# Performance work log

Measured on AMD Instinct MI355X. Metric: run time of the kernel, lower is better.

## Reference

```python
import jax, jax.numpy as jnp
import numpy as np


def setup_inputs() -> dict:
    key = jax.random.key(0)
    k1, k2, k3, k4 = jax.random.split(key, 4)
    B, T, S, D = 256, 16, 32, 768
    return {
        "video_global": jax.random.normal(k1, (B, D), dtype=jnp.float32),
        "text_global": jax.random.normal(k2, (B, D), dtype=jnp.float32),
        "video_local": jax.random.normal(k3, (B, T, D), dtype=jnp.float32),
        "text_local": jax.random.normal(k4, (B, S, D), dtype=jnp.float32),
        "temp": jnp.zeros((1,), dtype=jnp.float32),  # log(1.0)
    }


def reference(video_global, text_global, video_local, text_local, temp):
    B = video_global.shape[0]
    logit_scale = jnp.exp(temp)[0]

    # ---- global contrastive loss ----
    global_sim = logit_scale * (video_global @ text_global.T)  # [B, B]
    diag = jnp.arange(B)
    loss_v2t = -jax.nn.log_softmax(global_sim, axis=1)[diag, diag].mean()
    loss_t2v = -jax.nn.log_softmax(global_sim, axis=0)[diag, diag].mean()
    loss_global = 0.5 * (loss_v2t + loss_t2v)

    # ---- local positive scores ----
    # paired (diagonal) local similarity: [B, T, S]
    sim_pos = logit_scale * jnp.einsum("btd,bsd->bts", video_local, text_local)
    time_weights = jax.nn.softmax(sim_pos.max(axis=-1), axis=-1)  # [B, T]
    pos_scores = (sim_pos.mean(axis=-1) * time_weights).sum(axis=1)  # [B]

    # ---- local negative scores (batched pairwise contraction) ----
    # [B, B, T, S]: video i vs text j, replacing the B*(B-1) tiny einsum loop
    sim_all = logit_scale * jnp.einsum("btd,csd->bcts", video_local, text_local)
    neg_full = (time_weights[:, None, :] * sim_all.mean(axis=-1)).sum(axis=-1)  # [B, B]

    # drop diagonal (i == j), preserving row-major loop order
    rows, cols = np.nonzero(~np.eye(B, dtype=bool))
    neg_scores = neg_full[rows, cols].reshape(B, B - 1)

    logits = jnp.concatenate([pos_scores[:, None], neg_scores], axis=-1)  # [B, B]
    loss_local = -jax.nn.log_softmax(logits, axis=-1)[:, 0].mean()

    return 0.6 * loss_global + 0.4 * loss_local
```

## Files before the change

### kernel.cpp

```cpp
#include <hip/hip_runtime.h>
#include <cmath>

#define BB 256
#define TT 16
#define SS 32
#define DD 768
#define LROW 260

__global__ __launch_bounds__(256) void hl_stage1(
    const float* __restrict__ vl, const float* __restrict__ tl,
    const float* __restrict__ temp,
    float* __restrict__ vw_ws, float* __restrict__ tb_ws)
{
    __shared__ float smem[12480];
    const int i   = blockIdx.x;
    const int tid = threadIdx.x;
    const float lsc = expf(temp[0]);

    const int slice = tid >> 4;
    const int tpos  = (tid >> 2) & 3;
    const int spos  = tid & 3;

    const float* vli = vl + (size_t)i * TT * DD;
    const float* tli = tl + (size_t)i * SS * DD;

    float acc[4][8];
#pragma unroll
    for (int a0 = 0; a0 < 4; ++a0)
#pragma unroll
        for (int b0 = 0; b0 < 8; ++b0) acc[a0][b0] = 0.f;

    for (int c = 0; c < 3; ++c) {
        const int d0 = c << 8;
#pragma unroll
        for (int k = 0; k < 4; ++k) {
            int f4 = tid + (k << 8);
            int r  = f4 >> 6;
            int dc = (f4 << 2) & 255;
            *(float4*)&smem[r * LROW + dc] =
                *(const float4*)&vli[r * DD + d0 + dc];
        }
#pragma unroll
        for (int k = 0; k < 8; ++k) {
            int f4 = tid + (k << 8);
            int r  = f4 >> 6;
            int dc = (f4 << 2) & 255;
            *(float4*)&smem[(16 + r) * LROW + dc] =
                *(const float4*)&tli[r * DD + d0 + dc];
        }
        __syncthreads();
#pragma unroll
        for (int step = 0; step < 4; ++step) {
            const int db = (slice << 4) + (step << 2);
            float4 av[4];
            float4 bv[8];
#pragma unroll
            for (int ti = 0; ti < 4; ++ti)
                av[ti] = *(const float4*)&smem[(tpos * 4 + ti) * LROW + db];
#pragma unroll
            for (int sj = 0; sj < 8; ++sj)
                bv[sj] = *(const float4*)&smem[(16 + spos * 8 + sj) * LROW + db];
#pragma unroll
            for (int ti = 0; ti < 4; ++ti)
#pragma unroll
                for (int sj = 0; sj < 8; ++sj)
                    acc[ti][sj] += av[ti].x * bv[sj].x + av[ti].y * bv[sj].y
                                 + av[ti].z * bv[sj].z + av[ti].w * bv[sj].w;
        }
        __syncthreads();
    }

#pragma unroll
    for (int ti = 0; ti < 4; ++ti)
#pragma unroll
        for (int sj = 0; sj < 8; ++sj) {
            int t = tpos * 4 + ti, s = spos * 8 + sj;
            smem[(t * 32 + s) * 16 + slice] = acc[ti][sj];
        }
    __syncthreads();
    for (int rep = 0; rep < 2; ++rep) {
        int o = tid + (rep << 8);
        float ssum = 0.f;
#pragma unroll
        for (int k = 0; k < 16; ++k) ssum += smem[o * 16 + k];
        smem[8192 + o] = lsc * ssum;
    }
    __syncthreads();
    if (tid < 16) {
        float m = -3.0e38f;
        for (int s = 0; s < 32; ++s) m = fmaxf(m, smem[8192 + tid * 32 + s]);
        smem[8704 + tid] = m;
    }
    __syncthreads();
    if (tid == 0) {
        float M = -3.0e38f;
        for (int t = 0; t < 16; ++t) M = fmaxf(M, smem[8704 + t]);
        float ssum = 0.f;
        for (int t = 0; t < 16; ++t) {
            float e = expf(smem[8704 + t] - M);
            smem[8720 + t] = e;
            ssum += e;
        }
        float inv = 1.0f / ssum;
        for (int t = 0; t < 16; ++t) smem[8720 + t] *= inv;
    }
    __syncthreads();

#pragma unroll
    for (int k = 0; k < 3; ++k) {
        int d = tid + (k << 8);
        float vwv = 0.f;
#pragma unroll
        for (int t = 0; t < 16; ++t) vwv += smem[8720 + t] * vli[t * DD + d];
        vw_ws[(size_t)i * DD + d] = vwv;
        float tbv = 0.f;
#pragma unroll
        for (int s = 0; s < 32; ++s) tbv += tli[s * DD + d];
        tb_ws[(size_t)i * DD + d] = tbv * (1.0f / 32.0f);
    }
}

__global__ __launch_bounds__(256) void hl_stage2(
    const float* __restrict__ vg, const float* __restrict__ tg,
    const float* __restrict__ vw, const float* __restrict__ tb,
    const float* __restrict__ temp, float* __restrict__ out)
{
    __shared__ float a_s[4 * DD];
    __shared__ float xs[4 * 256];
    __shared__ float wred[4];
    __shared__ float bcast;

    const int tid  = threadIdx.x;
    const int mode = blockIdx.x >> 6;
    const int ib   = (blockIdx.x & 63) << 2;
    const float lsc = expf(temp[0]);

    const float* Arows;
    const float* Mat;
    float w;
    if (mode == 0)      { Arows = vw + (size_t)ib * DD; Mat = tb; w = 0.4f / 256.0f; }
    else if (mode == 1) { Arows = vg + (size_t)ib * DD; Mat = tg; w = 0.3f / 256.0f; }
    else                { Arows = tg + (size_t)ib * DD; Mat = vg; w = 0.3f / 256.0f; }

#pragma unroll
    for (int k = 0; k < 3; ++k) {
        int f4 = tid + (k << 8);
        *(float4*)&a_s[f4 << 2] = *(const float4*)&Arows[f4 << 2];
    }
    __syncthreads();

    const float4* mrow = (const float4*)(Mat + (size_t)tid * DD);
    float4 acc[4];
#pragma unroll
    for (int r = 0; r < 4; ++r) { acc[r].x = acc[r].y = acc[r].z = acc[r].w = 0.f; }

#pragma unroll 4
    for (int k = 0; k < DD / 4; ++k) {
        float4 m4 = mrow[k];
#pragma unroll
        for (int r = 0; r < 4; ++r) {
            float4 a4 = *(const float4*)&a_s[r * DD + (k << 2)];
            acc[r].x += m4.x * a4.x;
            acc[r].y += m4.y * a4.y;
            acc[r].z += m4.z * a4.z;
            acc[r].w += m4.w * a4.w;
        }
    }
#pragma unroll
    for (int r = 0; r < 4; ++r)
        xs[r * 256 + tid] = (acc[r].x + acc[r].y + acc[r].z + acc[r].w) * lsc;
    __syncthreads();

    float local = 0.f;
    for (int r = 0; r < 4; ++r) {
        float v = xs[r * 256 + tid];
        float m = v;
#pragma unroll
        for (int off = 32; off > 0; off >>= 1)
            m = fmaxf(m, __shfl_down(m, off, 64));
        if ((tid & 63) == 0) wred[tid >> 6] = m;
        __syncthreads();
        if (tid == 0)
            bcast = fmaxf(fmaxf(wred[0], wred[1]), fmaxf(wred[2], wred[3]));
        __syncthreads();
        float M = bcast;
        float e = expf(v - M);
        float ssum = e;
#pragma unroll
        for (int off = 32; off > 0; off >>= 1)
            ssum += __shfl_down(ssum, off, 64);
        if ((tid & 63) == 0) wred[tid >> 6] = ssum;
        __syncthreads();
        if (tid == 0) {
            float Stot = wred[0] + wred[1] + wred[2] + wred[3];
            float lse  = M + logf(Stot);
            local += w * (lse - xs[r * 256 + ib + r]);
        }
        __syncthreads();
    }
    if (tid == 0) atomicAdd(out, local);
}

extern "C" void kernel_launch(void* const* d_in, const int* in_sizes, int n_in,
                              void* d_out, int out_size, void* d_ws, size_t ws_size,
                              hipStream_t stream)
{
    const float* vg   = (const float*)d_in[0];
    const float* tg   = (const float*)d_in[1];
    const float* vl   = (const float*)d_in[2];
    const float* tl   = (const float*)d_in[3];
    const float* temp = (const float*)d_in[4];
    float* out = (float*)d_out;

    float* vw = (float*)d_ws;
    float* tb = vw + (size_t)BB * DD;

    hipMemsetAsync(out, 0, sizeof(float) * out_size, stream);
    hl_stage1<<<dim3(BB), dim3(256), 0, stream>>>(vl, tl, temp, vw, tb);
    hl_stage2<<<dim3(192), dim3(256), 0, stream>>>(vg, tg, vw, tb, temp, out);
}
```

Measured before the change: 125.1 us.

## Split-K tiled GEMM for global/local sims with separate LSE kernel, widen stage1

```diff
diff --git a/kernel.cpp b/kernel.cpp
--- a/kernel.cpp
+++ b/kernel.cpp
@@ -7,63 +7,65 @@
 #define DD 768
 #define LROW 260
 
-__global__ __launch_bounds__(256) void hl_stage1(
+__global__ __launch_bounds__(512) void hl_stage1(
     const float* __restrict__ vl, const float* __restrict__ tl,
     const float* __restrict__ temp,
     float* __restrict__ vw_ws, float* __restrict__ tb_ws)
 {
     __shared__ float smem[12480];
+    __shared__ float simb[512];
+    __shared__ float rmax[16];
+    __shared__ float twb[16];
+
     const int i   = blockIdx.x;
     const int tid = threadIdx.x;
     const float lsc = expf(temp[0]);
 
-    const int slice = tid >> 4;
-    const int tpos  = (tid >> 2) & 3;
-    const int spos  = tid & 3;
+    const int slice = tid & 15;
+    const int g     = tid >> 4;
+    const int tg    = g >> 3;
+    const int sg    = g & 7;
 
     const float* vli = vl + (size_t)i * TT * DD;
     const float* tli = tl + (size_t)i * SS * DD;
 
-    float acc[4][8];
-#pragma unroll
-    for (int a0 = 0; a0 < 4; ++a0)
-#pragma unroll
-        for (int b0 = 0; b0 < 8; ++b0) acc[a0][b0] = 0.f;
+    float acc[4][4];
+#pragma unroll
+    for (int a = 0; a < 4; ++a)
+#pragma unroll
+        for (int b = 0; b < 4; ++b) acc[a][b] = 0.f;
 
     for (int c = 0; c < 3; ++c) {
         const int d0 = c << 8;
 #pragma unroll
+        for (int k = 0; k < 2; ++k) {
+            int f4 = tid + (k << 9);
+            int r  = f4 >> 6;
+            int dc = (f4 & 63) << 2;
+            *(float4*)&smem[r * LROW + dc] = *(const float4*)&vli[r * DD + d0 + dc];
+        }
+#pragma unroll
         for (int k = 0; k < 4; ++k) {
-            int f4 = tid + (k << 8);
+            int f4 = tid + (k << 9);
             int r  = f4 >> 6;
-            int dc = (f4 << 2) & 255;
-            *(float4*)&smem[r * LROW + dc] =
-                *(const float4*)&vli[r * DD + d0 + dc];
-        }
-#pragma unroll
-        for (int k = 0; k < 8; ++k) {
-            int f4 = tid + (k << 8);
-            int r  = f4 >> 6;
-            int dc = (f4 << 2) & 255;
-            *(float4*)&smem[(16 + r) * LROW + dc] =
-                *(const float4*)&tli[r * DD + d0 + dc];
+            int dc = (f4 & 63) << 2;
+            *(float4*)&smem[(16 + r) * LROW + dc] = *(const float4*)&tli[r * DD + d0 + dc];
         }
         __syncthreads();
 #pragma unroll
         for (int step = 0; step < 4; ++step) {
             const int db = (slice << 4) + (step << 2);
-            float4 av[4];
-            float4 bv[8];
+            float4 av[4], bv[4];
 #pragma unroll
             for (int ti = 0; ti < 4; ++ti)
-                av[ti] = *(const float4*)&smem[(tpos * 4 + ti) * LROW + db];
-#pragma unroll
-            for (int sj = 0; sj < 8; ++sj)
-                bv[sj] = *(const float4*)&smem[(16 + spos * 8 + sj) * LROW + db];
+                av[ti] = *(const float4*)&smem[(tg * 4 + ti) * LROW + db];
+#pragma unroll
+            for (int sj = 0; sj < 4; ++sj)
+                bv[sj] = *(const float4*)&smem[(16 + sg * 4 + sj) * LROW + db];
 #pragma unroll
             for (int ti = 0; ti < 4; ++ti)
 #pragma unroll
-                for (int sj = 0; sj < 8; ++sj)
+                for (int sj = 0; sj < 4; ++sj)
                     acc[ti][sj] += av[ti].x * bv[sj].x + av[ti].y * bv[sj].y
                                  + av[ti].z * bv[sj].z + av[ti].w * bv[sj].w;
         }
@@ -73,45 +75,43 @@
 #pragma unroll
     for (int ti = 0; ti < 4; ++ti)
 #pragma unroll
-        for (int sj = 0; sj < 8; ++sj) {
-            int t = tpos * 4 + ti, s = spos * 8 + sj;
-            smem[(t * 32 + s) * 16 + slice] = acc[ti][sj];
-        }
-    __syncthreads();
-    for (int rep = 0; rep < 2; ++rep) {
-        int o = tid + (rep << 8);
+        for (int sj = 0; sj < 4; ++sj) {
+            int t = tg * 4 + ti, s = sg * 4 + sj;
+            smem[(t * 32 + s) * 17 + slice] = acc[ti][sj];
+        }
+    __syncthreads();
+    {
         float ssum = 0.f;
 #pragma unroll
-        for (int k = 0; k < 16; ++k) ssum += smem[o * 16 + k];
-        smem[8192 + o] = lsc * ssum;
+        for (int k = 0; k < 16; ++k) ssum += smem[tid * 17 + k];
+        simb[tid] = lsc * ssum;
     }
     __syncthreads();
     if (tid < 16) {
         float m = -3.0e38f;
-        for (int s = 0; s < 32; ++s) m = fmaxf(m, smem[8192 + tid * 32 + s]);
-        smem[8704 + tid] = m;
+        for (int s = 0; s < 32; ++s)
+            m = fmaxf(m, simb[tid * 32 + ((s + tid) & 31)]);
+        rmax[tid] = m;
     }
     __syncthreads();
     if (tid == 0) {
         float M = -3.0e38f;
-        for (int t = 0; t < 16; ++t) M = fmaxf(M, smem[8704 + t]);
+        for (int t = 0; t < 16; ++t) M = fmaxf(M, rmax[t]);
         float ssum = 0.f;
         for (int t = 0; t < 16; ++t) {
-            float e = expf(smem[8704 + t] - M);
-            smem[8720 + t] = e;
+            float e = expf(rmax[t] - M);
+            twb[t] = e;
             ssum += e;
         }
         float inv = 1.0f / ssum;
-        for (int t = 0; t < 16; ++t) smem[8720 + t] *= inv;
-    }
-    __syncthreads();
-
-#pragma unroll
-    for (int k = 0; k < 3; ++k) {
-        int d = tid + (k << 8);
+        for (int t = 0; t < 16; ++t) twb[t] *= inv;
+    }
+    __syncthreads();
+
+    for (int d = tid; d < DD; d += 512) {
         float vwv = 0.f;
 #pragma unroll
-        for (int t = 0; t < 16; ++t) vwv += smem[8720 + t] * vli[t * DD + d];
+        for (int t = 0; t < 16; ++t) vwv += twb[t] * vli[t * DD + d];
         vw_ws[(size_t)i * DD + d] = vwv;
         float tbv = 0.f;
 #pragma unroll
@@ -120,85 +120,124 @@
     }
 }
 
-__global__ __launch_bounds__(256) void hl_stage2(
+__global__ __launch_bounds__(256) void hl_gemm(
     const float* __restrict__ vg, const float* __restrict__ tg,
     const float* __restrict__ vw, const float* __restrict__ tb,
-    const float* __restrict__ temp, float* __restrict__ out)
-{
-    __shared__ float a_s[4 * DD];
-    __shared__ float xs[4 * 256];
+    const float* __restrict__ temp, float* __restrict__ cparts)
+{
+    __shared__ float As[16][68];
+    __shared__ float Bs[16][68];
+    __shared__ float Tb[64][68];
+
+    const int b   = blockIdx.x;
+    const int p   = b & 7;
+    const int tj  = (b >> 3) & 3;
+    const int ti  = (b >> 5) & 3;
+    const int mat = b >> 7;
+    const int tid = threadIdx.x;
+    const float lsc = expf(temp[0]);
+
+    const float* A  = mat ? vw : vg;
+    const float* Bm = mat ? tb : tg;
+    const int i0 = ti * 64, j0 = tj * 64, kb0 = p * 96;
+
+    const int srow = tid >> 2, skq = tid & 3;
+    const int tr = tid >> 4, tc = tid & 15;
+
+    float acc[4][4];
+#pragma unroll
+    for (int r = 0; r < 4; ++r)
+#pragma unroll
+        for (int cc = 0; cc < 4; ++cc) acc[r][cc] = 0.f;
+
+    for (int ch = 0; ch < 6; ++ch) {
+        const int kb = kb0 + ch * 16;
+        float4 a4 = *(const float4*)&A [(size_t)(i0 + srow) * DD + kb + skq * 4];
+        float4 b4 = *(const float4*)&Bm[(size_t)(j0 + srow) * DD + kb + skq * 4];
+        __syncthreads();
+        As[skq * 4 + 0][srow] = a4.x; As[skq * 4 + 1][srow] = a4.y;
+        As[skq * 4 + 2][srow] = a4.z; As[skq * 4 + 3][srow] = a4.w;
+        Bs[skq * 4 + 0][srow] = b4.x; Bs[skq * 4 + 1][srow] = b4.y;
+        Bs[skq * 4 + 2][srow] = b4.z; Bs[skq * 4 + 3][srow] = b4.w;
+        __syncthreads();
+#pragma unroll
+        for (int k = 0; k < 16; ++k) {
+            float4 av = *(const float4*)&As[k][tr * 4];
+            float4 bv = *(const float4*)&Bs[k][tc * 4];
+            float ar[4] = {av.x, av.y, av.z, av.w};
+            float br[4] = {bv.x, bv.y, bv.z, bv.w};
+#pragma unroll
+            for (int r = 0; r < 4; ++r)
+#pragma unroll
+                for (int cc = 0; cc < 4; ++cc)
+                    acc[r][cc] += ar[r] * br[cc];
+        }
+    }
+
+    const int cm = mat ? 0 : 1;
+    float* Cp = cparts + ((size_t)p * 3 + cm) * 65536;
+#pragma unroll
+    for (int r = 0; r < 4; ++r) {
+        float4 v = {acc[r][0] * lsc, acc[r][1] * lsc, acc[r][2] * lsc, acc[r][3] * lsc};
+        *(float4*)&Cp[(size_t)(i0 + tr * 4 + r) * 256 + j0 + tc * 4] = v;
+    }
+    if (mat == 0) {
+        __syncthreads();
+#pragma unroll
+        for (int r = 0; r < 4; ++r)
+#pragma unroll
+            for (int cc = 0; cc < 4; ++cc)
+                Tb[tc * 4 + cc][tr * 4 + r] = acc[r][cc] * lsc;
+        __syncthreads();
+        float* Ct = cparts + ((size_t)p * 3 + 2) * 65536;
+#pragma unroll
+        for (int r = 0; r < 4; ++r) {
+            float4 v = *(const float4*)&Tb[tr * 4 + r][tc * 4];
+            *(float4*)&Ct[(size_t)(j0 + tr * 4 + r) * 256 + i0 + tc * 4] = v;
+        }
+    }
+}
+
+__global__ __launch_bounds__(256) void hl_lse(
+    const float* __restrict__ cparts, float* __restrict__ out)
+{
+    __shared__ float xs[256];
     __shared__ float wred[4];
     __shared__ float bcast;
 
-    const int tid  = threadIdx.x;
-    const int mode = blockIdx.x >> 6;
-    const int ib   = (blockIdx.x & 63) << 2;
-    const float lsc = expf(temp[0]);
-
-    const float* Arows;
-    const float* Mat;
-    float w;
-    if (mode == 0)      { Arows = vw + (size_t)ib * DD; Mat = tb; w = 0.4f / 256.0f; }
-    else if (mode == 1) { Arows = vg + (size_t)ib * DD; Mat = tg; w = 0.3f / 256.0f; }
-    else                { Arows = tg + (size_t)ib * DD; Mat = vg; w = 0.3f / 256.0f; }
-
-#pragma unroll
-    for (int k = 0; k < 3; ++k) {
-        int f4 = tid + (k << 8);
-        *(float4*)&a_s[f4 << 2] = *(const float4*)&Arows[f4 << 2];
-    }
-    __syncthreads();
-
-    const float4* mrow = (const float4*)(Mat + (size_t)tid * DD);
-    float4 acc[4];
-#pragma unroll
-    for (int r = 0; r < 4; ++r) { acc[r].x = acc[r].y = acc[r].z = acc[r].w = 0.f; }
-
-#pragma unroll 4
-    for (int k = 0; k < DD / 4; ++k) {
-        float4 m4 = mrow[k];
-#pragma unroll
-        for (int r = 0; r < 4; ++r) {
-            float4 a4 = *(const float4*)&a_s[r * DD + (k << 2)];
-            acc[r].x += m4.x * a4.x;
-            acc[r].y += m4.y * a4.y;
-            acc[r].z += m4.z * a4.z;
-            acc[r].w += m4.w * a4.w;
-        }
-    }
-#pragma unroll
-    for (int r = 0; r < 4; ++r)
-        xs[r * 256 + tid] = (acc[r].x + acc[r].y + acc[r].z + acc[r].w) * lsc;
-    __syncthreads();
-
-    float local = 0.f;
-    for (int r = 0; r < 4; ++r) {
-        float v = xs[r * 256 + tid];
-        float m = v;
-#pragma unroll
-        for (int off = 32; off > 0; off >>= 1)
-            m = fmaxf(m, __shfl_down(m, off, 64));
-        if ((tid & 63) == 0) wred[tid >> 6] = m;
-        __syncthreads();
-        if (tid == 0)
-            bcast = fmaxf(fmaxf(wred[0], wred[1]), fmaxf(wred[2], wred[3]));
-        __syncthreads();
-        float M = bcast;
-        float e = expf(v - M);
-        float ssum = e;
-#pragma unroll
-        for (int off = 32; off > 0; off >>= 1)
-            ssum += __shfl_down(ssum, off, 64);
-        if ((tid & 63) == 0) wred[tid >> 6] = ssum;
-        __syncthreads();
-        if (tid == 0) {
-            float Stot = wred[0] + wred[1] + wred[2] + wred[3];
-            float lse  = M + logf(Stot);
-            local += w * (lse - xs[r * 256 + ib + r]);
-        }
-        __syncthreads();
-    }
-    if (tid == 0) atomicAdd(out, local);
+    const int b   = blockIdx.x;
+    const int cm  = b >> 8;
+    const int row = b & 255;
+    const int tid = threadIdx.x;
+
+    float x = 0.f;
+#pragma unroll
+    for (int p = 0; p < 8; ++p)
+        x += cparts[((size_t)p * 3 + cm) * 65536 + (size_t)row * 256 + tid];
+    xs[tid] = x;
+
+    float m = x;
+#pragma unroll
+    for (int off = 32; off > 0; off >>= 1)
+        m = fmaxf(m, __shfl_down(m, off, 64));
+    if ((tid & 63) == 0) wred[tid >> 6] = m;
+    __syncthreads();
+    if (tid == 0)
+        bcast = fmaxf(fmaxf(wred[0], wred[1]), fmaxf(wred[2], wred[3]));
+    __syncthreads();
+    float M = bcast;
+    float e = expf(x - M);
+#pragma unroll
+    for (int off = 32; off > 0; off >>= 1)
+        e += __shfl_down(e, off, 64);
+    if ((tid & 63) == 0) wred[tid >> 6] = e;
+    __syncthreads();
+    if (tid == 0) {
+        float Stot = wred[0] + wred[1] + wred[2] + wred[3];
+        float lse  = M + logf(Stot);
+        float w    = (cm == 0) ? (0.4f / 256.0f) : (0.3f / 256.0f);
+        atomicAdd(out, w * (lse - xs[row]));
+    }
 }
 
 extern "C" void kernel_launch(void* const* d_in, const int* in_sizes, int n_in,
@@ -212,10 +251,12 @@
     const float* temp = (const float*)d_in[4];
     float* out = (float*)d_out;
 
-    float* vw = (float*)d_ws;
-    float* tb = vw + (size_t)BB * DD;
+    float* vw     = (float*)d_ws;
+    float* tb     = vw + (size_t)BB * DD;
+    float* cparts = tb + (size_t)BB * DD;
 
     hipMemsetAsync(out, 0, sizeof(float) * out_size, stream);
-    hl_stage1<<<dim3(BB), dim3(256), 0, stream>>>(vl, tl, temp, vw, tb);
-    hl_stage2<<<dim3(192), dim3(256), 0, stream>>>(vg, tg, vw, tb, temp, out);
-}
+    hl_stage1<<<dim3(BB),  dim3(512), 0, stream>>>(vl, tl, temp, vw, tb);
+    hl_gemm  <<<dim3(256), dim3(256), 0, stream>>>(vg, tg, vw, tb, temp, cparts);
+    hl_lse   <<<dim3(768), dim3(256), 0, stream>>>(cparts, out);
+}
```

After: 118.0 us. 5.7% less time.
